# Kernel optimization log

Measured on AMD Instinct MI355X. Metric: run time of the kernel, lower is better.

The kernel has to match this reference:

```python
import jax, jax.numpy as jnp
import numpy as np

B, S, H = 2, 2048, 1024
E, K, F = 8, 2, 4096


def setup_inputs() -> dict:
    key = jax.random.key(0)
    ks = jax.random.split(key, 7)
    s_h = 1.0 / np.sqrt(H)
    s_f = 1.0 / np.sqrt(F)
    return {
        "hidden_states": jax.random.normal(ks[0], (B, S, H), jnp.float32),
        "Wr": jax.random.normal(ks[1], (H, E), jnp.float32) * s_h,
        "br": jnp.zeros((E,), jnp.float32),
        "W1": jax.random.normal(ks[2], (E, H, F), jnp.float32) * s_h,
        "b1": jnp.zeros((E, F), jnp.float32),
        "W2": jax.random.normal(ks[3], (E, F, H), jnp.float32) * s_f,
        "b2": jnp.zeros((E, H), jnp.float32),
    }


def _moe_forward(hidden_states, Wr, br, W1, b1, W2, b2):
    b, s, h = hidden_states.shape
    x = hidden_states.reshape(-1, h)  # [T, H]
    # --- router: top-k over softmax probs, renormalized ---
    logits = x @ Wr + br  # [T, E]
    probs = jax.nn.softmax(logits, axis=-1)
    top_w, top_i = jax.lax.top_k(probs, K)  # [T, K]
    weights = top_w / jnp.sum(top_w, axis=-1, keepdims=True)  # [T, K]
    # --- dense-equivalent expert dispatch + combine ---
    # per-token per-expert combine weight (zero for unselected experts)
    out = jnp.zeros_like(x)
    for e in range(E):
        w_e = jnp.sum(weights * (top_i == e), axis=-1)  # [T]
        h_e = jax.nn.gelu(x @ W1[e] + b1[e], approximate=False)  # [T, F]
        y_e = h_e @ W2[e] + b2[e]  # [T, H]
        out = out + w_e[:, None] * y_e
    # --- aux load-balance loss (counts are constants wrt grads) ---
    counts = jnp.sum(jax.nn.one_hot(top_i, E, dtype=logits.dtype), axis=(0, 1))  # [E]
    load = counts / (top_i.size)
    aux_loss = jnp.mean((load - 1.0 / E) ** 2)
    # --- z-loss ---
    z_loss = jnp.mean(jax.nn.logsumexp(logits, axis=-1))
    total_loss = 0.01 * aux_loss + 0.001 * z_loss
    return out.reshape(b, s, h), total_loss


def reference(hidden_states, Wr, br, W1, b1, W2, b2):
    output, total_loss = _moe_forward(hidden_states, Wr, br, W1, b1, W2, b2)
    return output, total_loss
```

## Files before the change

kernel.cpp:

```cpp
#include <hip/hip_runtime.h>
#include <stdint.h>
#include <math.h>

#define T_TOK 4096
#define H_DIM 1024
#define E_EXP 8
#define F_DIM 4096
#define NASSIGN (T_TOK * 2)
#define OUT_ELEMS ((size_t)T_TOK * H_DIM)
#define YB_ELEMS ((size_t)8192 * H_DIM)

typedef unsigned short u16;
typedef __attribute__((ext_vector_type(8))) short short8;
typedef __attribute__((ext_vector_type(4))) float f32x4;

__device__ __forceinline__ u16 f2bf(float f) {
  union { float f; uint32_t u; } c; c.f = f;
  uint32_t u = c.u;
  return (u16)((u + 0x7FFFu + ((u >> 16) & 1u)) >> 16);
}

__device__ __forceinline__ void gl_lds16(const void* g, void* l) {
  __builtin_amdgcn_global_load_lds(
      (const __attribute__((address_space(1))) uint32_t*)g,
      (__attribute__((address_space(3))) uint32_t*)(uintptr_t)l, 16, 0, 0);
}

__global__ __launch_bounds__(256) void transpose_cvt_tiled(
    const float* __restrict__ in, u16* __restrict__ out, int R, int C) {
  __shared__ u16 tile[64][72];
  const size_t eoff = (size_t)blockIdx.z * R * C;
  {
    const int c4 = (threadIdx.x & 15) * 4;
    const int rr = threadIdx.x >> 4;
    const float* inp = in + eoff + ((size_t)blockIdx.y * 64) * C + blockIdx.x * 64;
#pragma unroll
    for (int p = 0; p < 4; ++p) {
      const int r = rr + p * 16;
      const float4 v = *(const float4*)(inp + (size_t)r * C + c4);
      tile[r][c4 + 0] = f2bf(v.x); tile[r][c4 + 1] = f2bf(v.y);
      tile[r][c4 + 2] = f2bf(v.z); tile[r][c4 + 3] = f2bf(v.w);
    }
  }
  __syncthreads();
  {
    u16* op = out + (((size_t)blockIdx.z * (C >> 6) + blockIdx.x) * (R >> 6)
                     + blockIdx.y) * 4096;
#pragma unroll
    for (int p = 0; p < 2; ++p) {
      const int c = (threadIdx.x >> 3) + p * 32;
      const int rg = (threadIdx.x & 7) * 8;
      short8 o;
#pragma unroll
      for (int j = 0; j < 8; ++j) o[j] = (short)tile[rg + j][c];
      *(short8*)(op + c * 64 + rg) = o;
    }
  }
}

__global__ void router_kernel(const float* __restrict__ x, const float* __restrict__ Wr,
                              const float* __restrict__ br, u16* __restrict__ xb,
                              int* __restrict__ tki, float* __restrict__ tkw,
                              int* __restrict__ counts, float* __restrict__ zsum) {
  const int wave = threadIdx.x >> 6;
  const int lane = threadIdx.x & 63;
  __shared__ int lcnt[8];
  __shared__ float lzv[16];
  if (threadIdx.x < 8) lcnt[threadIdx.x] = 0;
  __syncthreads();
#pragma unroll
  for (int it = 0; it < 4; ++it) {
    const int t = blockIdx.x * 16 + wave * 4 + it;
    const float* xr = x + (size_t)t * H_DIM;
    u16* xbr = xb + (size_t)t * H_DIM;
    float acc[8];
#pragma unroll
    for (int e = 0; e < 8; ++e) acc[e] = 0.0f;
#pragma unroll
    for (int j = 0; j < 16; ++j) {
      const int hh = j * 64 + lane;
      const float xv = xr[hh];
      xbr[hh] = f2bf(xv);
      const float4 w0 = *(const float4*)(Wr + (size_t)hh * 8);
      const float4 w1 = *(const float4*)(Wr + (size_t)hh * 8 + 4);
      acc[0] += xv * w0.x; acc[1] += xv * w0.y; acc[2] += xv * w0.z; acc[3] += xv * w0.w;
      acc[4] += xv * w1.x; acc[5] += xv * w1.y; acc[6] += xv * w1.z; acc[7] += xv * w1.w;
    }
#pragma unroll
    for (int e = 0; e < 8; ++e) {
      float v = acc[e];
#pragma unroll
      for (int s = 32; s > 0; s >>= 1) v += __shfl_xor(v, s);
      acc[e] = v;
    }
    if (lane == 0) {
      float l[8];
#pragma unroll
      for (int e = 0; e < 8; ++e) l[e] = acc[e] + br[e];
      float mx = l[0];
#pragma unroll
      for (int e = 1; e < 8; ++e) mx = fmaxf(mx, l[e]);
      float p[8], s = 0.0f;
#pragma unroll
      for (int e = 0; e < 8; ++e) { p[e] = __expf(l[e] - mx); s += p[e]; }
      int i0 = 0;
#pragma unroll
      for (int e = 1; e < 8; ++e) if (p[e] > p[i0]) i0 = e;
      int i1 = (i0 == 0) ? 1 : 0;
#pragma unroll
      for (int e = 0; e < 8; ++e) if (e != i1 && e != i0 && p[e] > p[i1]) i1 = e;
      const float ws = p[i0] + p[i1];
      tki[2 * t] = i0; tki[2 * t + 1] = i1;
      tkw[2 * t] = p[i0] / ws; tkw[2 * t + 1] = p[i1] / ws;
      atomicAdd(&lcnt[i0], 1);
      atomicAdd(&lcnt[i1], 1);
      lzv[wave * 4 + it] = mx + logf(s);
    }
  }
  __syncthreads();
  if (threadIdx.x < 8) {
    const int c = lcnt[threadIdx.x];
    if (c) atomicAdd(&counts[threadIdx.x], c);
  }
  if (threadIdx.x == 64) {
    float zs = 0.0f;
#pragma unroll
    for (int i = 0; i < 16; ++i) zs += lzv[i];
    atomicAdd(zsum, zs);
  }
}

__global__ void scatter_kernel(const int* __restrict__ tki, const float* __restrict__ tkw,
                               const int* __restrict__ counts, int* __restrict__ cursor,
                               int* __restrict__ perm, float* __restrict__ pw,
                               int* __restrict__ islot,
                               const float* __restrict__ zsum, float* __restrict__ out_loss) {
  int offs[8];
  {
    int a = 0;
#pragma unroll
    for (int e = 0; e < 8; ++e) { offs[e] = a; a += counts[e]; }
  }
  const int lane = threadIdx.x & 63;
  const int t = blockIdx.x * 256 + threadIdx.x;
#pragma unroll
  for (int k = 0; k < 2; ++k) {
    const int e = tki[2 * t + k];
    int slot = 0;
#pragma unroll
    for (int ee = 0; ee < 8; ++ee) {
      const unsigned long long mask = __ballot(e == ee);
      if (mask) {
        const int leader = __ffsll(mask) - 1;
        int b = 0;
        if (lane == leader) b = atomicAdd(&cursor[ee], (int)__popcll(mask));
        b = __shfl(b, leader);
        if (e == ee) {
          const int r = (int)__popcll(mask & ((1ull << lane) - 1ull));
          slot = offs[ee] + b + r;
        }
      }
    }
    perm[slot] = t;
    pw[slot] = tkw[2 * t + k];
    islot[2 * t + k] = slot;
  }
  if (blockIdx.x == 0 && threadIdx.x == 0) {
    float aux = 0.0f;
#pragma unroll
    for (int e = 0; e < 8; ++e) {
      const float d = (float)counts[e] / (float)NASSIGN - 0.125f;
      aux += d * d;
    }
    aux *= (1.0f / 8.0f);
    out_loss[0] = 0.01f * aux + 0.001f * (zsum[0] / (float)T_TOK);
  }
}


__global__ __launch_bounds__(256, 4) void gemm1_kernel(
    const u16* __restrict__ xb, const u16* __restrict__ w1t,
    const float* __restrict__ b1, const int* __restrict__ perm,
    const int* __restrict__ cnts, u16* __restrict__ hbuf) {
  const int id = blockIdx.x;
  const int e = id & 7;
  const int wq = id >> 3;
  const int n0 = (wq & 31) << 7;
  const int m0 = (wq >> 5) << 7;
  int cnt, off;
  {
    int a = 0, c = 0;
#pragma unroll
    for (int i = 0; i < 8; ++i) { const int ci = cnts[i]; if (i < e) a += ci; if (i == e) c = ci; }
    cnt = c; off = a;
  }
  if (m0 >= cnt) return;

  __shared__ __align__(16) u16 smem[16384];
  u16* As = smem;
  u16* Bs = smem + 8192;

  const int tid = threadIdx.x;
  const int rbase = tid >> 3;
  const int kc = ((tid & 7) ^ (rbase & 7)) * 8;

  const u16* ap[4];
#pragma unroll
  for (int l = 0; l < 4; ++l) {
    int ra = m0 + rbase + l * 32; if (ra > cnt - 1) ra = cnt - 1;
    ap[l] = xb + (size_t)perm[off + ra] * H_DIM + kc;
  }
  const u16* bp0 = w1t + ((((size_t)e * (F_DIM >> 6) + (n0 >> 6)) * (H_DIM >> 6)) << 12)
                 + rbase * 64 + kc;
  const size_t bnt = (size_t)(H_DIM >> 6) << 12;

  const int wave = tid >> 6, lane = tid & 63;
  const int wm = (wave >> 1) * 64, wn = (wave & 1) * 64;
  const int lr = lane & 15, q = lane >> 4;
  const int qs0 = q ^ (lr & 7), qs1 = (4 + q) ^ (lr & 7);

  f32x4 acc[4][4];
#pragma unroll
  for (int i = 0; i < 4; ++i)
#pragma unroll
    for (int j = 0; j < 4; ++j) acc[i][j] = (f32x4)0.0f;

  const short8* Afr = (const short8*)As;
  const short8* Bfr = (const short8*)Bs;

  for (int k0 = 0; k0 < (H_DIM >> 6); ++k0) {
    gl_lds16(ap[0], &As[(size_t)tid * 8]);
    gl_lds16(ap[1], &As[(size_t)(tid + 256) * 8]);
    gl_lds16(ap[2], &As[(size_t)(tid + 512) * 8]);
    gl_lds16(ap[3], &As[(size_t)(tid + 768) * 8]);
    gl_lds16(bp0,              &Bs[(size_t)tid * 8]);
    gl_lds16(bp0 + 2048,       &Bs[(size_t)(tid + 256) * 8]);
    gl_lds16(bp0 + bnt,        &Bs[(size_t)(tid + 512) * 8]);
    gl_lds16(bp0 + bnt + 2048, &Bs[(size_t)(tid + 768) * 8]);
#pragma unroll
    for (int l = 0; l < 4; ++l) ap[l] += 64;
    bp0 += 4096;
    __syncthreads();
#pragma unroll
    for (int s = 0; s < 2; ++s) {
      const int qs = s ? qs1 : qs0;
      short8 a[4], b[4];
#pragma unroll
      for (int i = 0; i < 4; ++i) a[i] = Afr[(wm + i * 16 + lr) * 8 + qs];
#pragma unroll
      for (int j = 0; j < 4; ++j) b[j] = Bfr[(wn + j * 16 + lr) * 8 + qs];
#pragma unroll
      for (int i = 0; i < 4; ++i)
#pragma unroll
        for (int j = 0; j < 4; ++j)
          acc[i][j] = __builtin_amdgcn_mfma_f32_16x16x32_bf16(a[i], b[j], acc[i][j], 0, 0, 0);
    }
    __syncthreads();
  }

#pragma unroll
  for (int i = 0; i < 4; ++i) {
#pragma unroll
    for (int rr = 0; rr < 4; ++rr) {
      const int row = wm + i * 16 + q * 4 + rr;
#pragma unroll
      for (int j = 0; j < 4; ++j) {
        const int col = wn + j * 16 + lr;
        const float v = acc[i][j][rr] + b1[e * F_DIM + n0 + col];
        const float g = 0.5f * v * (1.0f + erff(v * 0.70710678118654752f));
        smem[(row << 7) + (col ^ (q << 4))] = f2bf(g);
      }
    }
  }
  __syncthreads();
#pragma unroll
  for (int p = 0; p < 8; ++p) {
    const int ml = p * 16 + (tid >> 4);
    const int nl = (tid & 15) * 8;
    const int m = m0 + ml;
    if (m < cnt) {
      const int qq = (ml >> 2) & 3;
      *(short8*)(hbuf + (size_t)(off + m) * F_DIM + n0 + nl) =
          *(const short8*)(smem + (ml << 7) + (nl ^ (qq << 4)));
    }
  }
}

__global__ __launch_bounds__(256, 4) void gemm2_kernel(
    const u16* __restrict__ hbuf, const u16* __restrict__ w2t,
    const float* __restrict__ b2, const float* __restrict__ pw,
    const int* __restrict__ cnts, float* __restrict__ ybuf) {
  const int id = blockIdx.x;
  const int e = id & 7;
  const int wq = id >> 3;
  const int n0 = (wq & 7) << 7;
  const int ks = (wq >> 3) & 1;
  const int m0 = (wq >> 4) << 7;
  int cnt, off;
  {
    int a = 0, c = 0;
#pragma unroll
    for (int i = 0; i < 8; ++i) { const int ci = cnts[i]; if (i < e) a += ci; if (i == e) c = ci; }
    cnt = c; off = a;
  }
  if (m0 >= cnt) return;

  __shared__ __align__(16) u16 As[128 * 64];
  __shared__ __align__(16) u16 Bs[128 * 64];

  const int tid = threadIdx.x;
  const int rbase = tid >> 3;
  const int kc = ((tid & 7) ^ (rbase & 7)) * 8;

  const u16* ap[4];
#pragma unroll
  for (int l = 0; l < 4; ++l) {
    int ra = m0 + rbase + l * 32; if (ra > cnt - 1) ra = cnt - 1;
    ap[l] = hbuf + (size_t)(off + ra) * F_DIM + (ks << 11) + kc;
  }
  const u16* bp0 = w2t + ((((size_t)e * (H_DIM >> 6) + (n0 >> 6)) * (F_DIM >> 6)) << 12)
                 + ((size_t)(ks << 5) << 12) + rbase * 64 + kc;
  const size_t bnt = (size_t)(F_DIM >> 6) << 12;

  const int wave = tid >> 6, lane = tid & 63;
  const int wm = (wave >> 1) * 64, wn = (wave & 1) * 64;
  const int lr = lane & 15, q = lane >> 4;
  const int qs0 = q ^ (lr & 7), qs1 = (4 + q) ^ (lr & 7);

  f32x4 acc[4][4];
#pragma unroll
  for (int i = 0; i < 4; ++i)
#pragma unroll
    for (int j = 0; j < 4; ++j) acc[i][j] = (f32x4)0.0f;

  const short8* Afr = (const short8*)As;
  const short8* Bfr = (const short8*)Bs;

  for (int k0 = 0; k0 < 32; ++k0) {
    gl_lds16(ap[0], &As[(size_t)tid * 8]);
    gl_lds16(ap[1], &As[(size_t)(tid + 256) * 8]);
    gl_lds16(ap[2], &As[(size_t)(tid + 512) * 8]);
    gl_lds16(ap[3], &As[(size_t)(tid + 768) * 8]);
    gl_lds16(bp0,              &Bs[(size_t)tid * 8]);
    gl_lds16(bp0 + 2048,       &Bs[(size_t)(tid + 256) * 8]);
    gl_lds16(bp0 + bnt,        &Bs[(size_t)(tid + 512) * 8]);
    gl_lds16(bp0 + bnt + 2048, &Bs[(size_t)(tid + 768) * 8]);
#pragma unroll
    for (int l = 0; l < 4; ++l) ap[l] += 64;
    bp0 += 4096;
    __syncthreads();
#pragma unroll
    for (int s = 0; s < 2; ++s) {
      const int qs = s ? qs1 : qs0;
      short8 a[4], b[4];
#pragma unroll
      for (int i = 0; i < 4; ++i) a[i] = Afr[(wm + i * 16 + lr) * 8 + qs];
#pragma unroll
      for (int j = 0; j < 4; ++j) b[j] = Bfr[(wn + j * 16 + lr) * 8 + qs];
#pragma unroll
      for (int i = 0; i < 4; ++i)
#pragma unroll
        for (int j = 0; j < 4; ++j)
          acc[i][j] = __builtin_amdgcn_mfma_f32_16x16x32_bf16(a[i], b[j], acc[i][j], 0, 0, 0);
    }
    __syncthreads();
  }

  float* yb = ybuf + (size_t)ks * YB_ELEMS;
#pragma unroll
  for (int i = 0; i < 4; ++i) {
#pragma unroll
    for (int rr = 0; rr < 4; ++rr) {
      const int m = m0 + wm + i * 16 + q * 4 + rr;
      if (m < cnt) {
        const int slot = off + m;
        const float w = pw[slot];
        float* orow = yb + (size_t)slot * H_DIM;
#pragma unroll
        for (int j = 0; j < 4; ++j) {
          const int col = n0 + wn + j * 16 + lr;
          float y = acc[i][j][rr];
          if (ks == 0) y += b2[e * H_DIM + col];
          orow[col] = w * y;
        }
      }
    }
  }
}

__global__ __launch_bounds__(256) void combine_kernel(
    const float* __restrict__ ybuf, const int* __restrict__ islot,
    float* __restrict__ out) {
  const int t = blockIdx.x;
  const int s0 = islot[2 * t];
  const int s1 = islot[2 * t + 1];
  const int c = threadIdx.x * 4;
  const float4 a0 = *(const float4*)(ybuf + (size_t)s0 * H_DIM + c);
  const float4 a1 = *(const float4*)(ybuf + YB_ELEMS + (size_t)s0 * H_DIM + c);
  const float4 b0 = *(const float4*)(ybuf + (size_t)s1 * H_DIM + c);
  const float4 b1 = *(const float4*)(ybuf + YB_ELEMS + (size_t)s1 * H_DIM + c);
  float4 r;
  r.x = a0.x + a1.x + b0.x + b1.x;
  r.y = a0.y + a1.y + b0.y + b1.y;
  r.z = a0.z + a1.z + b0.z + b1.z;
  r.w = a0.w + a1.w + b0.w + b1.w;
  *(float4*)(out + (size_t)t * H_DIM + c) = r;
}


extern "C" void kernel_launch(void* const* d_in, const int* in_sizes, int n_in,
                              void* d_out, int out_size, void* d_ws, size_t ws_size,
                              hipStream_t stream) {
  const float* x  = (const float*)d_in[0];
  const float* Wr = (const float*)d_in[1];
  const float* br = (const float*)d_in[2];
  const float* W1 = (const float*)d_in[3];
  const float* b1 = (const float*)d_in[4];
  const float* W2 = (const float*)d_in[5];
  const float* b2 = (const float*)d_in[6];
  float* out = (float*)d_out;

  char* ws = (char*)d_ws;
  u16* xb    = (u16*)(ws);
  u16* w1t   = (u16*)(ws + 8388608ull);
  u16* w2t   = (u16*)(ws + 75497472ull);
  u16* hbuf  = (u16*)(ws + 142606336ull);
  float* ybuf = (float*)(ws + 8388608ull);
  int*   tki    = (int*)(ws + 209715200ull);
  float* tkw    = (float*)(ws + 209747968ull);
  int*   perm   = (int*)(ws + 209780736ull);
  float* pw     = (float*)(ws + 209813504ull);
  int*   counts = (int*)(ws + 209846272ull);
  int*   cursor = counts + 8;
  float* zsum   = (float*)(counts + 16);
  int*   islot  = (int*)(ws + 209846400ull);

  hipMemsetAsync(counts, 0, 128, stream);

  transpose_cvt_tiled<<<dim3(F_DIM / 64, H_DIM / 64, E_EXP), 256, 0, stream>>>(W1, w1t, H_DIM, F_DIM);
  transpose_cvt_tiled<<<dim3(H_DIM / 64, F_DIM / 64, E_EXP), 256, 0, stream>>>(W2, w2t, F_DIM, H_DIM);
  router_kernel<<<T_TOK / 16, 256, 0, stream>>>(x, Wr, br, xb, tki, tkw, counts, zsum);
  scatter_kernel<<<T_TOK / 256, 256, 0, stream>>>(tki, tkw, counts, cursor, perm, pw,
                                                  islot, zsum, out + OUT_ELEMS);
  gemm1_kernel<<<8192, 256, 0, stream>>>(xb, w1t, b1, perm, counts, hbuf);
  gemm2_kernel<<<4096, 256, 0, stream>>>(hbuf, w2t, b2, pw, counts, ybuf);
  combine_kernel<<<T_TOK, 256, 0, stream>>>(ybuf, islot, out);
}
```

Before: 608.1 us.

## Fuse weight transposes with router, vectorize router loads, use polynomial erf

Merges the two weight transpose/convert launches and the router kernel into one prep kernel whose blocks pick a role from the block index, removing two launches and the tail gaps between them. The router now loads x as float4 and stores bf16 in packed 4-element writes. GELU's erff is replaced by an Abramowitz-Stegun style polynomial with a fast reciprocal and exp. That approximation has an absolute error around 1e-7 and is applied before bf16 rounding, but it is still less exact than erff.

```diff
diff --git a/kernel.cpp b/kernel.cpp
--- a/kernel.cpp
+++ b/kernel.cpp
@@ -12,6 +12,7 @@
 
 typedef unsigned short u16;
 typedef __attribute__((ext_vector_type(8))) short short8;
+typedef __attribute__((ext_vector_type(4))) short short4v;
 typedef __attribute__((ext_vector_type(4))) float f32x4;
 
 __device__ __forceinline__ u16 f2bf(float f) {
@@ -20,20 +21,33 @@
   return (u16)((u + 0x7FFFu + ((u >> 16) & 1u)) >> 16);
 }
 
+__device__ __forceinline__ float fast_erf(float u) {
+  const float au = fabsf(u);
+  const float t = __builtin_amdgcn_rcpf(__builtin_fmaf(0.3275911f, au, 1.0f));
+  float p = __builtin_fmaf(1.061405429f, t, -1.453152027f);
+  p = __builtin_fmaf(p, t, 1.421413741f);
+  p = __builtin_fmaf(p, t, -0.284496736f);
+  p = __builtin_fmaf(p, t, 0.254829592f);
+  p = p * t;
+  const float y = __builtin_fmaf(-p, __expf(-au * au), 1.0f);
+  return copysignf(y, u);
+}
+
 __device__ __forceinline__ void gl_lds16(const void* g, void* l) {
   __builtin_amdgcn_global_load_lds(
       (const __attribute__((address_space(1))) uint32_t*)g,
       (__attribute__((address_space(3))) uint32_t*)(uintptr_t)l, 16, 0, 0);
 }
 
-__global__ __launch_bounds__(256) void transpose_cvt_tiled(
-    const float* __restrict__ in, u16* __restrict__ out, int R, int C) {
-  __shared__ u16 tile[64][72];
-  const size_t eoff = (size_t)blockIdx.z * R * C;
+
+__device__ __forceinline__ void transpose_tile(
+    const float* __restrict__ in, u16* __restrict__ out, int R, int C,
+    int bx, int by, int bz, u16 (*tile)[72]) {
+  const size_t eoff = (size_t)bz * R * C;
   {
     const int c4 = (threadIdx.x & 15) * 4;
     const int rr = threadIdx.x >> 4;
-    const float* inp = in + eoff + ((size_t)blockIdx.y * 64) * C + blockIdx.x * 64;
+    const float* inp = in + eoff + ((size_t)by * 64) * C + bx * 64;
 #pragma unroll
     for (int p = 0; p < 4; ++p) {
       const int r = rr + p * 16;
@@ -44,8 +58,7 @@
   }
   __syncthreads();
   {
-    u16* op = out + (((size_t)blockIdx.z * (C >> 6) + blockIdx.x) * (R >> 6)
-                     + blockIdx.y) * 4096;
+    u16* op = out + (((size_t)bz * (C >> 6) + bx) * (R >> 6) + by) * 4096;
 #pragma unroll
     for (int p = 0; p < 2; ++p) {
       const int c = (threadIdx.x >> 3) + p * 32;
@@ -58,33 +71,58 @@
   }
 }
 
-__global__ void router_kernel(const float* __restrict__ x, const float* __restrict__ Wr,
-                              const float* __restrict__ br, u16* __restrict__ xb,
-                              int* __restrict__ tki, float* __restrict__ tkw,
-                              int* __restrict__ counts, float* __restrict__ zsum) {
+__global__ __launch_bounds__(256) void prep_kernel(
+    const float* __restrict__ x, const float* __restrict__ Wr,
+    const float* __restrict__ br, u16* __restrict__ xb,
+    int* __restrict__ tki, float* __restrict__ tkw,
+    int* __restrict__ counts, float* __restrict__ zsum,
+    const float* __restrict__ W1, u16* __restrict__ w1t,
+    const float* __restrict__ W2, u16* __restrict__ w2t) {
+  __shared__ u16 tile[64][72];
+  __shared__ int lcnt[8];
+  __shared__ float lzv[16];
+  const int id = blockIdx.x;
+
+  if (id >= 256) {
+    if (id < 8448) {
+      const int q = id - 256;
+      transpose_tile(W1, w1t, H_DIM, F_DIM, q & 63, (q >> 6) & 15, q >> 10, tile);
+    } else {
+      const int q = id - 8448;
+      transpose_tile(W2, w2t, F_DIM, H_DIM, q & 15, (q >> 4) & 63, q >> 10, tile);
+    }
+    return;
+  }
+
   const int wave = threadIdx.x >> 6;
   const int lane = threadIdx.x & 63;
-  __shared__ int lcnt[8];
-  __shared__ float lzv[16];
   if (threadIdx.x < 8) lcnt[threadIdx.x] = 0;
   __syncthreads();
 #pragma unroll
   for (int it = 0; it < 4; ++it) {
-    const int t = blockIdx.x * 16 + wave * 4 + it;
+    const int t = id * 16 + wave * 4 + it;
     const float* xr = x + (size_t)t * H_DIM;
     u16* xbr = xb + (size_t)t * H_DIM;
     float acc[8];
 #pragma unroll
     for (int e = 0; e < 8; ++e) acc[e] = 0.0f;
 #pragma unroll
-    for (int j = 0; j < 16; ++j) {
-      const int hh = j * 64 + lane;
-      const float xv = xr[hh];
-      xbr[hh] = f2bf(xv);
-      const float4 w0 = *(const float4*)(Wr + (size_t)hh * 8);
-      const float4 w1 = *(const float4*)(Wr + (size_t)hh * 8 + 4);
-      acc[0] += xv * w0.x; acc[1] += xv * w0.y; acc[2] += xv * w0.z; acc[3] += xv * w0.w;
-      acc[4] += xv * w1.x; acc[5] += xv * w1.y; acc[6] += xv * w1.z; acc[7] += xv * w1.w;
+    for (int j = 0; j < 4; ++j) {
+      const int h0 = j * 256 + lane * 4;
+      const float4 xv = *(const float4*)(xr + h0);
+      const float vv[4] = {xv.x, xv.y, xv.z, xv.w};
+      short4v pk;
+#pragma unroll
+      for (int i = 0; i < 4; ++i) {
+        pk[i] = (short)f2bf(vv[i]);
+        const float4 w0 = *(const float4*)(Wr + (size_t)(h0 + i) * 8);
+        const float4 w1 = *(const float4*)(Wr + (size_t)(h0 + i) * 8 + 4);
+        acc[0] += vv[i] * w0.x; acc[1] += vv[i] * w0.y;
+        acc[2] += vv[i] * w0.z; acc[3] += vv[i] * w0.w;
+        acc[4] += vv[i] * w1.x; acc[5] += vv[i] * w1.y;
+        acc[6] += vv[i] * w1.z; acc[7] += vv[i] * w1.w;
+      }
+      *(short4v*)(xbr + h0) = pk;
     }
 #pragma unroll
     for (int e = 0; e < 8; ++e) {
@@ -267,7 +305,7 @@
       for (int j = 0; j < 4; ++j) {
         const int col = wn + j * 16 + lr;
         const float v = acc[i][j][rr] + b1[e * F_DIM + n0 + col];
-        const float g = 0.5f * v * (1.0f + erff(v * 0.70710678118654752f));
+        const float g = 0.5f * v * (1.0f + fast_erf(v * 0.70710678118654752f));
         smem[(row << 7) + (col ^ (q << 4))] = f2bf(g);
       }
     }
@@ -437,9 +475,8 @@
 
   hipMemsetAsync(counts, 0, 128, stream);
 
-  transpose_cvt_tiled<<<dim3(F_DIM / 64, H_DIM / 64, E_EXP), 256, 0, stream>>>(W1, w1t, H_DIM, F_DIM);
-  transpose_cvt_tiled<<<dim3(H_DIM / 64, F_DIM / 64, E_EXP), 256, 0, stream>>>(W2, w2t, F_DIM, H_DIM);
-  router_kernel<<<T_TOK / 16, 256, 0, stream>>>(x, Wr, br, xb, tki, tkw, counts, zsum);
+  prep_kernel<<<16640, 256, 0, stream>>>(x, Wr, br, xb, tki, tkw, counts, zsum,
+                                         W1, w1t, W2, w2t);
   scatter_kernel<<<T_TOK / 256, 256, 0, stream>>>(tki, tkw, counts, cursor, perm, pw,
                                                   islot, zsum, out + OUT_ELEMS);
   gemm1_kernel<<<8192, 256, 0, stream>>>(xb, w1t, b1, perm, counts, hbuf);
```

After: 608.9 us. Within noise of the previous version (+0.1%).
